# Kernel optimization log

Measured on AMD Instinct MI355X. Metric: run time of the kernel, lower is better.

The kernel has to match this reference:

```python
import jax, jax.numpy as jnp
import numpy as np

N = 100000
E = 1600000
IN_DIM = 128
HID_DIM = 128
OUT_DIM = 128


def _gcn_conv(x, W, b, row, col, n):
    # PyG GCNConv: x' = D^{-1/2} (A + I) D^{-1/2} (x W) + b, self-loops included
    xw = x @ W  # [n, dout]
    deg = jnp.zeros((n,), xw.dtype).at[col].add(1.0)  # in-degree incl self-loops
    dinv = jnp.where(deg > 0, jax.lax.rsqrt(deg), 0.0)
    norm = dinv[row] * dinv[col]  # [e]
    msg = xw[row] * norm[:, None]  # [e, dout] -- dominant memory traffic
    out = jax.ops.segment_sum(msg, col, num_segments=n)
    return out + b


def setup_inputs() -> dict:
    key = jax.random.key(0)
    k1, k2, k3, k4, k5, k6 = jax.random.split(key, 6)
    posts = jax.random.normal(k1, (N, IN_DIM), dtype=jnp.float32)
    edge_index = jax.random.randint(k2, (2, E), 0, N, dtype=jnp.int64)
    W1 = jax.random.normal(k3, (IN_DIM, HID_DIM), dtype=jnp.float32) * (1.0 / np.sqrt(IN_DIM))
    b1 = jnp.zeros((HID_DIM,), dtype=jnp.float32)
    W2 = jax.random.normal(k4, (HID_DIM + IN_DIM, OUT_DIM), dtype=jnp.float32) * (1.0 / np.sqrt(HID_DIM + IN_DIM))
    b2 = jnp.zeros((OUT_DIM,), dtype=jnp.float32)
    return {"posts": posts, "W1": W1, "b1": b1, "W2": W2, "b2": b2,
            "edge_index": edge_index, "rootIndex": 0}


def reference(posts, W1, b1, W2, b2, edge_index, rootIndex):
    n = posts.shape[0]
    loops = jnp.arange(n, dtype=edge_index.dtype)
    row = jnp.concatenate([edge_index[0], loops])
    col = jnp.concatenate([edge_index[1], loops])

    conv1_out = _gcn_conv(posts, W1, b1, row, col, n)  # [n, hid]
    post_root = jnp.broadcast_to(posts[rootIndex], (n, posts.shape[1]))
    conv1_root = jnp.broadcast_to(conv1_out[rootIndex], (n, conv1_out.shape[1]))

    conv2_in = jax.nn.relu(jnp.concatenate([conv1_out, post_root], axis=1))
    # dropout is identity at inference
    conv2_out = jax.nn.relu(_gcn_conv(conv2_in, W2, b2, row, col, n))

    feature = jnp.concatenate([conv1_root, conv2_out], axis=1)  # [n, hid+out]
    # avg_pool1d(kernel_size=3, stride=1) over the feature axis -> [n, hid+out-2]
    pooled = (feature[:, :-2] + feature[:, 1:-1] + feature[:, 2:]) * (1.0 / 3.0)
    return pooled
```

## Files before the change

kernel.cpp:

```cpp
#include <hip/hip_runtime.h>
#include <hip/hip_fp16.h>

#define DIM 128
typedef _Float16 half8 __attribute__((ext_vector_type(8)));
typedef float f32x4 __attribute__((ext_vector_type(4)));

__global__ void k_scan1(const int* __restrict__ cnt, int* __restrict__ off,
                        int* __restrict__ bsum, int N){
  __shared__ int s[256];
  int i = blockIdx.x*256 + threadIdx.x;
  int v = (i < N) ? cnt[i] : 0;
  s[threadIdx.x] = v;
  __syncthreads();
  for (int d = 1; d < 256; d <<= 1){
    int t = (threadIdx.x >= d) ? s[threadIdx.x - d] : 0;
    __syncthreads();
    s[threadIdx.x] += t;
    __syncthreads();
  }
  if (i < N) off[i] = s[threadIdx.x] - v;
  if (threadIdx.x == 255) bsum[blockIdx.x] = s[255];
}

__global__ void k_scan2(int* __restrict__ bsum, int nb){
  __shared__ int s[512];
  int t = threadIdx.x;
  int v = (t < nb) ? bsum[t] : 0;
  s[t] = v;
  __syncthreads();
  for (int d = 1; d < 512; d <<= 1){
    int x = (t >= d) ? s[t - d] : 0;
    __syncthreads();
    s[t] += x;
    __syncthreads();
  }
  if (t < nb) bsum[t] = s[t] - v;
}

__global__ void k_scan3(int* __restrict__ off, const int* __restrict__ bsum,
                        const int* __restrict__ cnt, float* __restrict__ dinv,
                        __half* __restrict__ dinvh, int N){
  int i = blockIdx.x*blockDim.x + threadIdx.x;
  if (i < N){
    off[i] += bsum[i >> 8];
    float d = rsqrtf((float)(cnt[i] + 1));
    dinv[i] = d;
    dinvh[i] = __float2half_rn(d);
  }
}

#define NSTRIPE 8
__global__ void k_scatter(const int* __restrict__ row, const int* __restrict__ col,
                          const int* __restrict__ rank, const int* __restrict__ off,
                          int* __restrict__ pos, int* __restrict__ csr_row, int E, int N){
  int stride = gridDim.x * 256;
  int tid0 = blockIdx.x*256 + threadIdx.x;
  int hi0  = (int)(((long long)1 * N) / NSTRIPE);
  int pHi0 = off[hi0];
  for (int e = tid0; e < E; e += stride){
    int p = off[col[e]] + rank[e];
    pos[e] = p;
    if (p < pHi0) csr_row[p] = row[e];
  }
  for (int s = 1; s < NSTRIPE; s++){
    int lo = (int)(((long long)s * N) / NSTRIPE);
    int hi = (int)(((long long)(s+1) * N) / NSTRIPE);
    int pLo = off[lo];
    int pHi = (s == NSTRIPE-1) ? E : off[hi];
    for (int e = tid0; e < E; e += stride){
      int p = pos[e];
      if (p >= pLo && p < pHi) csr_row[p] = row[e];
    }
  }
}

__global__ void k_wprep(const float* __restrict__ W1, const float* __restrict__ W2,
                        __half* __restrict__ Wf1h, __half* __restrict__ Wf2h){
  const float* Wsrc = (blockIdx.x < 8) ? W1 : W2;
  _Float16* Wf = (_Float16*)((blockIdx.x < 8) ? Wf1h : Wf2h);
  int id   = (blockIdx.x & 7)*256 + threadIdx.x;
  int lane = id & 63;
  int ckc  = id >> 6;
  int kc   = ckc & 3, ct = ckc >> 2;
  int kbase = kc*32 + (lane >> 4)*8;
  int c     = ct*16 + (lane & 15);
  half8 v;
  #pragma unroll
  for (int i = 0; i < 8; i++)
    v[i] = (_Float16)Wsrc[(size_t)(kbase + i)*DIM + c];
  *(half8*)(Wf + (size_t)id*8) = v;
}

template<int INH>
__device__ __forceinline__ void gemm_mfma(const void* __restrict__ Xv,
    const _Float16* __restrict__ Wf, const float* __restrict__ addvec,
    const float* __restrict__ dinv, __half* __restrict__ Yh, int N, int doRelu, int gb){
  int wid = threadIdx.x >> 6;
  int l   = threadIdx.x & 63;
  int g   = l >> 4;
  int lr  = l & 15;
  int rowA = gb*64 + wid*16 + lr;
  int rA   = (rowA < N) ? rowA : (N - 1);

  f32x4 acc[8];
  #pragma unroll
  for (int ct = 0; ct < 8; ct++) acc[ct] = (f32x4){0.f, 0.f, 0.f, 0.f};

  #pragma unroll
  for (int kc = 0; kc < 4; kc++){
    half8 a;
    if (INH){
      a = *(const half8*)((const _Float16*)Xv + (size_t)rA*DIM + kc*32 + g*8);
    } else {
      const float* xp = (const float*)Xv + (size_t)rA*DIM + kc*32 + g*8;
      float4 x0 = *(const float4*)xp;
      float4 x1 = *(const float4*)(xp + 4);
      a[0]=(_Float16)x0.x; a[1]=(_Float16)x0.y; a[2]=(_Float16)x0.z; a[3]=(_Float16)x0.w;
      a[4]=(_Float16)x1.x; a[5]=(_Float16)x1.y; a[6]=(_Float16)x1.z; a[7]=(_Float16)x1.w;
    }
    if (doRelu){
      #pragma unroll
      for (int i = 0; i < 8; i++) a[i] = (a[i] > (_Float16)0.f) ? a[i] : (_Float16)0.f;
    }
    #pragma unroll
    for (int ct = 0; ct < 8; ct++){
      half8 b = *(const half8*)(Wf + ((size_t)(ct*4 + kc)*64 + l)*8);
      acc[ct] = __builtin_amdgcn_mfma_f32_16x16x32_f16(a, b, acc[ct], 0, 0, 0);
    }
  }

  int m0 = gb*64 + wid*16 + g*4;
  float av[8];
  #pragma unroll
  for (int ct = 0; ct < 8; ct++) av[ct] = addvec ? addvec[ct*16 + lr] : 0.f;
  #pragma unroll
  for (int r = 0; r < 4; r++){
    int rr = m0 + r;
    if (rr < N){
      float dv = dinv ? dinv[rr] : 1.f;
      #pragma unroll
      for (int ct = 0; ct < 8; ct++){
        float o = dv*(acc[ct][r] + av[ct]);
        Yh[(size_t)rr*DIM + ct*16 + lr] = __float2half(o);
      }
    }
  }
}

__global__ __launch_bounds__(256) void k_megaA(const float* __restrict__ posts,
    const __half* __restrict__ Wf1, __half* __restrict__ xw1u,
    const int* __restrict__ col, int E, int* __restrict__ cnt, int* __restrict__ rank,
    int N, int nG, int nC){
  int bid = blockIdx.x;
  int m = bid % 5;
  if (m == 4){
    int g = bid / 5;
    if (g < nG)
      gemm_mfma<0>(posts, (const _Float16*)Wf1, nullptr, nullptr, xw1u, N, 0, g);
  } else {
    int c = (bid/5)*4 + m;
    if (c < nC){
      int i = c*256 + threadIdx.x;
      if (i < E) rank[i] = atomicAdd(&cnt[col[i]], 1);
    }
  }
}

__global__ __launch_bounds__(256) void k_megaC(const __half* __restrict__ c1h,
    const __half* __restrict__ Wf2, const float* __restrict__ cvec,
    const float* __restrict__ dinv, __half* __restrict__ xw2s,
    const float* __restrict__ cpool, float* __restrict__ outp, int N, int nG, int nF){
  int bid = blockIdx.x;
  if (bid < nG){
    gemm_mfma<1>(c1h, (const _Float16*)Wf2, cvec, dinv, xw2s, N, 1, bid);
  } else {
    int f = bid - nG;
    if (f >= nF) return;
    int total = N * 63;
    #pragma unroll
    for (int i = 0; i < 8; i++){
      int w = f*2048 + i*256 + threadIdx.x;
      if (w < total){
        unsigned int r  = (unsigned int)w / 63u;
        unsigned int c2 = (unsigned int)w - r*63u;
        float2 val = *(const float2*)(cpool + c2*2);
        *(float2*)(outp + (size_t)r*254 + c2*2) = val;
      }
    }
  }
}

__global__ void k_conv1(const __half* __restrict__ xw1u, const int* __restrict__ csr_row,
                        const int* __restrict__ off, const int* __restrict__ cnt,
                        const float* __restrict__ dinv, const __half* __restrict__ dinvh,
                        const float* __restrict__ b, const int* __restrict__ rootIdx,
                        __half* __restrict__ outh, float* __restrict__ c1root, int N){
  int wid  = (blockIdx.x*blockDim.x + threadIdx.x) >> 6;
  if (wid >= N) return;
  int lane = threadIdx.x & 63;
  int half = lane >> 5;
  int sl   = lane & 31;
  int v = wid;
  float dv = dinv[v];
  int o0 = off[v], total = cnt[v] + 1;

  __half2 a01 = __float2half2_rn(0.f), a23 = __float2half2_rn(0.f);
  const __half* base = xw1u;

  auto idx = [&](int t){ return (t == 0) ? v : csr_row[o0 + t - 1]; };
  auto accum = [&](uint2 wv, __half dh){
    __half2 d2 = __half2half2(dh);
    a01 = __hfma2(*(__half2*)&wv.x, d2, a01);
    a23 = __hfma2(*(__half2*)&wv.y, d2, a23);
  };

  int j = half;
  if (j + 14 < total){
    int nid[8];
    #pragma unroll
    for (int q = 0; q < 8; q++) nid[q] = idx(j + 2*q);
    while (j + 14 < total){
      int cur[8];
      #pragma unroll
      for (int q = 0; q < 8; q++) cur[q] = nid[q];
      int jn = j + 16;
      if (jn + 14 < total){
        #pragma unroll
        for (int q = 0; q < 8; q++) nid[q] = csr_row[o0 + jn + 2*q - 1];
      }
      uint2 u[8]; __half dh[8];
      #pragma unroll
      for (int q = 0; q < 8; q++){
        u[q]  = *(const uint2*)(base + (size_t)cur[q]*DIM + sl*4);
        dh[q] = dinvh[cur[q]];
      }
      #pragma unroll
      for (int q = 0; q < 8; q++) accum(u[q], dh[q]);
      j = jn;
    }
  }
  while (j + 6 < total){
    int i0 = idx(j), i1 = idx(j+2), i2 = idx(j+4), i3 = idx(j+6);
    uint2 u0 = *(const uint2*)(base + (size_t)i0*DIM + sl*4);
    uint2 u1 = *(const uint2*)(base + (size_t)i1*DIM + sl*4);
    uint2 u2 = *(const uint2*)(base + (size_t)i2*DIM + sl*4);
    uint2 u3 = *(const uint2*)(base + (size_t)i3*DIM + sl*4);
    __half d0 = dinvh[i0], d1 = dinvh[i1], d2 = dinvh[i2], d3 = dinvh[i3];
    accum(u0, d0); accum(u1, d1); accum(u2, d2); accum(u3, d3);
    j += 8;
  }
  for (; j < total; j += 2){
    int r = idx(j);
    uint2 u = *(const uint2*)(base + (size_t)r*DIM + sl*4);
    accum(u, dinvh[r]);
  }

  int r01 = __shfl_xor(*(int*)&a01, 32);
  int r23 = __shfl_xor(*(int*)&a23, 32);
  a01 = __hadd2(a01, *(__half2*)&r01);
  a23 = __hadd2(a23, *(__half2*)&r23);

  if (half == 0){
    float2 f01 = __half22float2(a01), f23 = __half22float2(a23);
    float4 bb = *(const float4*)(b + sl*4);
    float rx = dv*f01.x + bb.x, ry = dv*f01.y + bb.y;
    float rz = dv*f23.x + bb.z, rw = dv*f23.y + bb.w;
    __half2 h01 = __floats2half2_rn(rx, ry);
    __half2 h23 = __floats2half2_rn(rz, rw);
    uint2 u = make_uint2(*(unsigned int*)&h01, *(unsigned int*)&h23);
    *(uint2*)(outh + (size_t)v*DIM + sl*4) = u;
    if (v == rootIdx[0])
      *(float4*)(c1root + sl*4) = make_float4(rx, ry, rz, rw);
  }
}

__global__ void k_small(const float* __restrict__ posts, const float* __restrict__ W2,
                        const float* __restrict__ c1root, const int* __restrict__ rootIdx,
                        float* __restrict__ cvec, float* __restrict__ cpool){
  int j = threadIdx.x;
  int root = rootIdx[0];
  __shared__ float pr[DIM];
  __shared__ float cr[DIM];
  pr[j] = fmaxf(posts[(size_t)root*DIM + j], 0.f);
  cr[j] = c1root[j];
  __syncthreads();
  float s = 0.f;
  #pragma unroll 4
  for (int k = 0; k < DIM; k++) s += pr[k] * W2[(size_t)(DIM + k)*DIM + j];
  cvec[j] = s;
  cpool[j] = (j < 126) ? (cr[j] + cr[j+1] + cr[j+2]) * (1.f/3.f) : cr[j];
}

__global__ void k_conv2(const __half* __restrict__ xws, const int* __restrict__ csr_row,
                        const int* __restrict__ off, const int* __restrict__ cnt,
                        const float* __restrict__ dinv, const float* __restrict__ b2,
                        const float* __restrict__ cpool, float* __restrict__ out, int N){
  int wid  = (blockIdx.x*blockDim.x + threadIdx.x) >> 6;
  if (wid >= N) return;
  int lane = threadIdx.x & 63;
  int half = lane >> 5;
  int sl   = lane & 31;
  int v = wid;
  float dv = dinv[v];
  int o0 = off[v], total = cnt[v] + 1;

  __half2 a01 = __float2half2_rn(0.f), a23 = __float2half2_rn(0.f);
  const __half* base = xws;

  auto idx = [&](int t){ return (t == 0) ? v : csr_row[o0 + t - 1]; };
  auto accum = [&](uint2 wv){
    a01 = __hadd2(a01, *(__half2*)&wv.x);
    a23 = __hadd2(a23, *(__half2*)&wv.y);
  };

  int j = half;
  if (j + 14 < total){
    int nid[8];
    #pragma unroll
    for (int q = 0; q < 8; q++) nid[q] = idx(j + 2*q);
    while (j + 14 < total){
      int cur[8];
      #pragma unroll
      for (int q = 0; q < 8; q++) cur[q] = nid[q];
      int jn = j + 16;
      if (jn + 14 < total){
        #pragma unroll
        for (int q = 0; q < 8; q++) nid[q] = csr_row[o0 + jn + 2*q - 1];
      }
      uint2 u[8];
      #pragma unroll
      for (int q = 0; q < 8; q++) u[q] = *(const uint2*)(base + (size_t)cur[q]*DIM + sl*4);
      #pragma unroll
      for (int q = 0; q < 8; q++) accum(u[q]);
      j = jn;
    }
  }
  while (j + 6 < total){
    int i0 = idx(j), i1 = idx(j+2), i2 = idx(j+4), i3 = idx(j+6);
    uint2 u0 = *(const uint2*)(base + (size_t)i0*DIM + sl*4);
    uint2 u1 = *(const uint2*)(base + (size_t)i1*DIM + sl*4);
    uint2 u2 = *(const uint2*)(base + (size_t)i2*DIM + sl*4);
    uint2 u3 = *(const uint2*)(base + (size_t)i3*DIM + sl*4);
    accum(u0); accum(u1); accum(u2); accum(u3);
    j += 8;
  }
  for (; j < total; j += 2){
    uint2 u = *(const uint2*)(base + (size_t)idx(j)*DIM + sl*4);
    accum(u);
  }

  int r01 = __shfl_xor(*(int*)&a01, 32);
  int r23 = __shfl_xor(*(int*)&a23, 32);
  a01 = __hadd2(a01, *(__half2*)&r01);
  a23 = __hadd2(a23, *(__half2*)&r23);

  if (half == 0){
    float2 f01 = __half22float2(a01), f23 = __half22float2(a23);
    float4 bb = *(const float4*)(b2 + sl*4);
    float o0v = fmaxf(dv*f01.x + bb.x, 0.f);
    float o1v = fmaxf(dv*f01.y + bb.y, 0.f);
    float o2v = fmaxf(dv*f23.x + bb.z, 0.f);
    float o3v = fmaxf(dv*f23.y + bb.w, 0.f);

    float pz = __shfl_up(o2v, 1);
    float pw = __shfl_up(o3v, 1);
    if (sl == 0){ pz = cpool[126]; pw = cpool[127]; }
    const float third = 1.f/3.f;
    float q0 = (pz + pw + o0v) * third;
    float q1 = (pw + o0v + o1v) * third;
    float q2 = (o0v + o1v + o2v) * third;
    float q3 = (o1v + o2v + o3v) * third;

    float* orow = out + (size_t)v*254;
    *(float2*)(orow + 126 + sl*4)     = make_float2(q0, q1);
    *(float2*)(orow + 126 + sl*4 + 2) = make_float2(q2, q3);
  }
}

extern "C" void kernel_launch(void* const* d_in, const int* in_sizes, int n_in,
                              void* d_out, int out_size, void* d_ws, size_t ws_size,
                              hipStream_t stream){
  const float* posts = (const float*)d_in[0];
  const float* W1    = (const float*)d_in[1];
  const float* b1    = (const float*)d_in[2];
  const float* W2    = (const float*)d_in[3];
  const float* b2    = (const float*)d_in[4];
  const int*   eidx  = (const int*)d_in[5];
  const int*   rootI = (const int*)d_in[6];
  int N = in_sizes[0] / DIM;
  int E = in_sizes[5] / 2;
  const int* row = eidx;
  const int* col = eidx + E;

  char* p = (char*)d_ws;
  auto alloc = [&](size_t bytes)->void*{
    void* q = (void*)p; p += (bytes + 255) & ~(size_t)255; return q;
  };
  __half* xw1u  = (__half*)alloc((size_t)N*DIM*2);
  __half* xw2s  = (__half*)alloc((size_t)N*DIM*2);
  __half* c1h   = (__half*)alloc((size_t)N*DIM*2);
  __half* Wf1   = (__half*)alloc((size_t)DIM*DIM*2);
  __half* Wf2   = (__half*)alloc((size_t)DIM*DIM*2);
  __half* dinvh = (__half*)alloc((size_t)N*2);
  float* dinv   = (float*)alloc((size_t)N*4);
  float* c1root = (float*)alloc(DIM*4);
  float* cvec   = (float*)alloc(DIM*4);
  float* cpool  = (float*)alloc(DIM*4);
  int*   cnt    = (int*)alloc((size_t)N*4);
  int*   off    = (int*)alloc((size_t)N*4);
  int*   rank   = (int*)alloc((size_t)E*4);
  int*   pos    = (int*)alloc((size_t)E*4);
  int*   bsum   = (int*)alloc(512*4);
  int*   csrrow = (int*)alloc((size_t)E*4);

  hipMemsetAsync(cnt, 0, (size_t)N*4, stream);

  int nb = (N + 255) / 256;
  int nG = (N + 63) / 64;
  int nC = (E + 255) / 256;
  int q5 = nG > (nC + 3)/4 ? nG : (nC + 3)/4;
  int nF = (N*63 + 2047) / 2048;

  k_wprep<<<16, 256, 0, stream>>>(W1, W2, Wf1, Wf2);
  k_megaA<<<5*q5, 256, 0, stream>>>(posts, Wf1, xw1u, col, E, cnt, rank, N, nG, nC);
  k_scan1<<<nb, 256, 0, stream>>>(cnt, off, bsum, N);
  k_scan2<<<1, 512, 0, stream>>>(bsum, nb);
  k_scan3<<<nb, 256, 0, stream>>>(off, bsum, cnt, dinv, dinvh, N);
  k_scatter<<<2048, 256, 0, stream>>>(row, col, rank, off, pos, csrrow, E, N);

  k_conv1<<<(N + 3)/4, 256, 0, stream>>>(xw1u, csrrow, off, cnt, dinv, dinvh, b1, rootI,
                                         c1h, c1root, N);
  k_small<<<1, 128, 0, stream>>>(posts, W2, c1root, rootI, cvec, cpool);
  k_megaC<<<nG + nF, 256, 0, stream>>>(c1h, Wf2, cvec, dinv, xw2s, cpool,
                                       (float*)d_out, N, nG, nF);
  k_conv2<<<(N + 3)/4, 256, 0, stream>>>(xw2s, csrrow, off, cnt, dinv, b2, cpool,
                                         (float*)d_out, N);
}
```

Measured before the change: 298.0 us.

## Privatize degree-count atomics into eight replica counter arrays

Degree counting now spreads its atomics across eight replicated per-node counter arrays, picked by block id, so that concurrent atomics on the same node contend less. The scan kernel folds the replicas into per-replica base offsets and the total count, and the scatter adds the replica base when computing each edge's CSR position. The block interleave in megaA also changes from 4 count blocks per GEMM block to 1:1 with 2*nC blocks. In exchange there is an 8x larger counter memset, extra reads and writes of base8 in the scan, and an extra gather in the scatter.

```diff
diff --git a/kernel.cpp b/kernel.cpp
--- a/kernel.cpp
+++ b/kernel.cpp
@@ -5,11 +5,23 @@
 typedef _Float16 half8 __attribute__((ext_vector_type(8)));
 typedef float f32x4 __attribute__((ext_vector_type(4)));
 
-__global__ void k_scan1(const int* __restrict__ cnt, int* __restrict__ off,
+__global__ void k_scan1(const int* __restrict__ cnt8, int* __restrict__ cnt,
+                        int* __restrict__ base8, int* __restrict__ off,
                         int* __restrict__ bsum, int N){
   __shared__ int s[256];
   int i = blockIdx.x*256 + threadIdx.x;
-  int v = (i < N) ? cnt[i] : 0;
+  int v = 0;
+  if (i < N){
+    int b = 0;
+    #pragma unroll
+    for (int x = 0; x < 8; x++){
+      int cx = cnt8[(size_t)x*N + i];
+      base8[(size_t)x*N + i] = b;
+      b += cx;
+    }
+    v = b;
+    cnt[i] = v;
+  }
   s[threadIdx.x] = v;
   __syncthreads();
   for (int d = 1; d < 256; d <<= 1){
@@ -52,13 +64,16 @@
 #define NSTRIPE 8
 __global__ void k_scatter(const int* __restrict__ row, const int* __restrict__ col,
                           const int* __restrict__ rank, const int* __restrict__ off,
+                          const int* __restrict__ base8,
                           int* __restrict__ pos, int* __restrict__ csr_row, int E, int N){
   int stride = gridDim.x * 256;
   int tid0 = blockIdx.x*256 + threadIdx.x;
   int hi0  = (int)(((long long)1 * N) / NSTRIPE);
   int pHi0 = off[hi0];
   for (int e = tid0; e < E; e += stride){
-    int p = off[col[e]] + rank[e];
+    int c = col[e];
+    int x = (2*(e >> 8) + 1) & 7;
+    int p = off[c] + base8[(size_t)x*N + c] + rank[e];
     pos[e] = p;
     if (p < pHi0) csr_row[p] = row[e];
   }
@@ -149,19 +164,20 @@
 
 __global__ __launch_bounds__(256) void k_megaA(const float* __restrict__ posts,
     const __half* __restrict__ Wf1, __half* __restrict__ xw1u,
-    const int* __restrict__ col, int E, int* __restrict__ cnt, int* __restrict__ rank,
-    int N, int nG, int nC){
+    const int* __restrict__ col, int E, int* __restrict__ cnt8, int* __restrict__ rank,
+    int N, int nG){
   int bid = blockIdx.x;
-  int m = bid % 5;
-  if (m == 4){
-    int g = bid / 5;
+  if ((bid & 1) == 0){
+    int g = bid >> 1;
     if (g < nG)
       gemm_mfma<0>(posts, (const _Float16*)Wf1, nullptr, nullptr, xw1u, N, 0, g);
   } else {
-    int c = (bid/5)*4 + m;
-    if (c < nC){
-      int i = c*256 + threadIdx.x;
-      if (i < E) rank[i] = atomicAdd(&cnt[col[i]], 1);
+    int cb = bid >> 1;
+    int i = cb*256 + threadIdx.x;
+    if (i < E){
+      int c = col[i];
+      int x = bid & 7;
+      rank[i] = atomicAdd(&cnt8[(size_t)x*N + c], 1);
     }
   }
 }
@@ -406,6 +422,8 @@
   float* c1root = (float*)alloc(DIM*4);
   float* cvec   = (float*)alloc(DIM*4);
   float* cpool  = (float*)alloc(DIM*4);
+  int*   cnt8   = (int*)alloc((size_t)8*N*4);
+  int*   base8  = (int*)alloc((size_t)8*N*4);
   int*   cnt    = (int*)alloc((size_t)N*4);
   int*   off    = (int*)alloc((size_t)N*4);
   int*   rank   = (int*)alloc((size_t)E*4);
@@ -413,20 +431,19 @@
   int*   bsum   = (int*)alloc(512*4);
   int*   csrrow = (int*)alloc((size_t)E*4);
 
-  hipMemsetAsync(cnt, 0, (size_t)N*4, stream);
+  hipMemsetAsync(cnt8, 0, (size_t)8*N*4, stream);
 
   int nb = (N + 255) / 256;
   int nG = (N + 63) / 64;
   int nC = (E + 255) / 256;
-  int q5 = nG > (nC + 3)/4 ? nG : (nC + 3)/4;
   int nF = (N*63 + 2047) / 2048;
 
   k_wprep<<<16, 256, 0, stream>>>(W1, W2, Wf1, Wf2);
-  k_megaA<<<5*q5, 256, 0, stream>>>(posts, Wf1, xw1u, col, E, cnt, rank, N, nG, nC);
-  k_scan1<<<nb, 256, 0, stream>>>(cnt, off, bsum, N);
+  k_megaA<<<2*nC, 256, 0, stream>>>(posts, Wf1, xw1u, col, E, cnt8, rank, N, nG);
+  k_scan1<<<nb, 256, 0, stream>>>(cnt8, cnt, base8, off, bsum, N);
   k_scan2<<<1, 512, 0, stream>>>(bsum, nb);
   k_scan3<<<nb, 256, 0, stream>>>(off, bsum, cnt, dinv, dinvh, N);
-  k_scatter<<<2048, 256, 0, stream>>>(row, col, rank, off, pos, csrrow, E, N);
+  k_scatter<<<2048, 256, 0, stream>>>(row, col, rank, off, base8, pos, csrrow, E, N);
 
   k_conv1<<<(N + 3)/4, 256, 0, stream>>>(xw1u, csrrow, off, cnt, dinv, dinvh, b1, rootI,
                                          c1h, c1root, N);
```

Result: no change. 300.8 us (+0.9%).
